# Optimization experiments

Hardware: AMD Instinct MI355X
Metric: run time of the kernel (lower is better)

Reference implementation:

```python
import jax, jax.numpy as jnp
import numpy as np

LOC_SIZE, LOC_EMB = 50000, 512
TIM_SIZE, TIM_EMB = 48, 32
UID_SIZE, UID_EMB = 10000, 64
HID = 512
H = HID + TIM_EMB  # 544, odeblock / merge width
N_SEG = 8192
TOTAL = 262144  # sum(history_count)
SEQ = 1024
TLEN = 1024


def setup_inputs() -> dict:
    key = jax.random.key(0)
    ks = jax.random.split(key, 12)
    # history_count: positive ints summing exactly to TOTAL
    rs = np.random.RandomState(0)
    counts = np.full(N_SEG, TOTAL // N_SEG, dtype=np.int32)  # 32 each
    d = rs.randint(0, 16, N_SEG // 2).astype(np.int32)
    counts[: N_SEG // 2] += d
    counts[N_SEG // 2 :] -= d  # min 17, sum preserved
    return {
        "loc": jax.random.randint(ks[0], (SEQ, 1), 0, LOC_SIZE, dtype=jnp.int32),
        "tim": jax.random.randint(ks[1], (SEQ, 1), 0, TIM_SIZE, dtype=jnp.int32),
        "history_loc": jax.random.randint(ks[2], (TOTAL, 1), 0, LOC_SIZE, dtype=jnp.int32),
        "history_tim": jax.random.randint(ks[3], (TOTAL, 1), 0, TIM_SIZE, dtype=jnp.int32),
        "history_count": jnp.asarray(counts),
        "uid": jax.random.randint(ks[4], (1,), 0, UID_SIZE, dtype=jnp.int32),
        "target_len": TLEN,
        "emb_loc_w": jax.random.normal(ks[5], (LOC_SIZE, LOC_EMB), jnp.float32) * 0.02,
        "emb_tim_w": jax.random.normal(ks[6], (TIM_SIZE, TIM_EMB), jnp.float32) * 0.02,
        "emb_uid_w": jax.random.normal(ks[7], (UID_SIZE, UID_EMB), jnp.float32) * 0.02,
        "gru_w": jax.random.normal(ks[8], (3, H, H), jnp.float32) * (1.0 / np.sqrt(H)),
        "gru_b": jnp.zeros((3, H), jnp.float32),
        "fc_final_w": jax.random.normal(ks[9], (H + UID_EMB, LOC_SIZE), jnp.float32) * 0.02,
        "fc_final_b": jnp.zeros((LOC_SIZE,), jnp.float32),
    }


def reference(loc, tim, history_loc, history_tim, history_count, uid, target_len,
              emb_loc_w, emb_tim_w, emb_uid_w, gru_w, gru_b, fc_final_w, fc_final_b):
    # ----- short-term sequence: embed, concat, dot-attention (Attn method='dot') -----
    x = jnp.concatenate([emb_loc_w[loc[:, 0]], emb_tim_w[tim[:, 0]]], axis=-1)  # [S, H]
    x = x[-target_len:]
    attn_w = jax.nn.softmax(x @ x.T, axis=-1)          # vectorized double-loop of Attn
    x_attn = attn_w @ x                                # [T, H]

    # ----- long-term history: variable-length segment mean (the python loop) -----
    loc_eh = emb_loc_w[history_loc[:, 0]]              # [TOTAL, LOC_EMB]
    tim_eh = emb_tim_w[history_tim[:, 0]]              # [TOTAL, TIM_EMB]
    csum = jnp.cumsum(history_count)                   # inclusive offsets
    offsets = csum - history_count                     # segment starts
    seg_ids = jnp.searchsorted(csum, jnp.arange(loc_eh.shape[0]), side="right")
    loc_mean = jax.ops.segment_sum(loc_eh, seg_ids, num_segments=history_count.shape[0])
    loc_mean = loc_mean / history_count[:, None].astype(x.dtype)  # [N_SEG, LOC_EMB]
    tim_first = tim_eh[offsets]                        # first tim of each segment
    history = jnp.concatenate([loc_mean, tim_first], axis=1)      # [N_SEG, H]

    # ----- merge, autonomous GRU-ODE block (single Euler step, dt=1) -----
    h = jnp.concatenate([history, x_attn], axis=0)     # [N_SEG+T, H]
    r = jax.nn.sigmoid(h @ gru_w[0] + gru_b[0])
    z = jax.nn.sigmoid(h @ gru_w[1] + gru_b[1])
    g = jnp.tanh((r * h) @ gru_w[2] + gru_b[2])
    out_state = h + (1.0 - z) * (g - h)                # h + dh (GRU-ODE derivative)

    # ----- output head -----
    out = out_state[-target_len:]
    uid_emb = jnp.broadcast_to(emb_uid_w[uid[0]], (target_len, emb_uid_w.shape[1]))
    y = jnp.concatenate([out, uid_emb], axis=1) @ fc_final_w + fc_final_b  # [T, V]
    return jax.nn.log_softmax(y, axis=-1)
```

## Files before the change

### kernel.cpp

```cpp
#include <hip/hip_runtime.h>
#include <hip/hip_bf16.h>
#include <math.h>

#define SEQ   1024
#define TL    1024
#define DLOC  512
#define DTIM  32
#define DH    544
#define DUID  64
#define DF    608
#define NVOC  50000
#define NT_FINAL 391
#define NPAD  50048

typedef __attribute__((ext_vector_type(8))) short short8;
typedef __attribute__((ext_vector_type(4))) float f32x4;
typedef __attribute__((ext_vector_type(4))) unsigned short u16x4;

#define WAITV8 asm volatile("s_waitcnt vmcnt(8)" ::: "memory")
#define WAITV4 asm volatile("s_waitcnt vmcnt(4)" ::: "memory")
#define WAITV0 asm volatile("s_waitcnt vmcnt(0)" ::: "memory")

__device__ __forceinline__ unsigned short f2bf(float f) {
    union { float f; unsigned int u; } x; x.f = f;
    unsigned int u = x.u;
    return (unsigned short)((u + 0x7fffu + ((u >> 16) & 1u)) >> 16);
}

__device__ __forceinline__ void gll16(const unsigned short* g, unsigned short* l) {
    __builtin_amdgcn_global_load_lds(
        (const __attribute__((address_space(1))) void*)g,
        (__attribute__((address_space(3))) void*)l,
        16, 0, 0);
}

enum { EPI_S = 0, EPI_PV = 1, EPI_G1 = 2, EPI_G2 = 3 };

template<int EPI>
__global__ __launch_bounds__(256) void gemm_p(
    const unsigned short* __restrict__ A,
    const unsigned short* __restrict__ Bt,
    int K, int N, int lda, int ldo,
    float* __restrict__ o1, unsigned short* __restrict__ o2,
    const float* __restrict__ p1, const float* __restrict__ p2,
    const float* __restrict__ p3, const float* __restrict__ p4)
{
    __shared__ __align__(16) unsigned short SMEM[32768];
    const int m0 = blockIdx.y << 7, n0 = blockIdx.x << 7;
    const int tid = threadIdx.x, w = tid >> 6, lane = tid & 63;
    const int wr = (w >> 1) << 6, wc = (w & 1) << 6;
    const int llo = lane & 15, lhi = lane >> 4;

    const int ch0 = (w * 2 + 0) * 64 + lane;
    const int ch1 = (w * 2 + 1) * 64 + lane;
    const int r0 = ch0 >> 2, s0 = (ch0 & 3) ^ ((r0 >> 1) & 3);
    const int r1 = ch1 >> 2, s1 = (ch1 & 3) ^ ((r1 >> 1) & 3);

    f32x4 acc[4][4];
    #pragma unroll
    for (int i = 0; i < 4; ++i)
        #pragma unroll
        for (int j = 0; j < 4; ++j)
            #pragma unroll
            for (int q = 0; q < 4; ++q) acc[i][j][q] = 0.0f;

    auto STAGE = [&](int buf, int kt) {
        const int k0 = kt << 5;
        unsigned short* As = &SMEM[buf * 4096];
        unsigned short* Bs = &SMEM[16384 + buf * 4096];
        gll16(&A [(size_t)(m0 + r0) * lda + k0 + s0 * 8], &As[(w * 2 + 0) * 512]);
        gll16(&A [(size_t)(m0 + r1) * lda + k0 + s1 * 8], &As[(w * 2 + 1) * 512]);
        gll16(&Bt[(size_t)(n0 + r0) * K   + k0 + s0 * 8], &Bs[(w * 2 + 0) * 512]);
        gll16(&Bt[(size_t)(n0 + r1) * K   + k0 + s1 * 8], &Bs[(w * 2 + 1) * 512]);
    };

    const int nk = K >> 5;
    STAGE(0, 0); STAGE(1, 1); STAGE(2, 2);
    WAITV8;
    __builtin_amdgcn_s_barrier();

    for (int t = 0; t < nk; ++t) {
        const unsigned short* As = &SMEM[(t & 3) * 4096];
        const unsigned short* Bs = &SMEM[16384 + (t & 3) * 4096];
        short8 af[4], bfv[4];
        #pragma unroll
        for (int fm = 0; fm < 4; ++fm) {
            int row = wr + fm * 16 + llo;
            af[fm] = *reinterpret_cast<const short8*>(&As[row * 32 + (lhi ^ ((row >> 1) & 3)) * 8]);
        }
        #pragma unroll
        for (int fn = 0; fn < 4; ++fn) {
            int row = wc + fn * 16 + llo;
            bfv[fn] = *reinterpret_cast<const short8*>(&Bs[row * 32 + (lhi ^ ((row >> 1) & 3)) * 8]);
        }
        if (t + 3 < nk) STAGE((t + 3) & 3, t + 3);
        __builtin_amdgcn_s_setprio(1);
        #pragma unroll
        for (int fm = 0; fm < 4; ++fm)
            #pragma unroll
            for (int fn = 0; fn < 4; ++fn)
                acc[fm][fn] = __builtin_amdgcn_mfma_f32_16x16x32_bf16(af[fm], bfv[fn], acc[fm][fn], 0, 0, 0);
        __builtin_amdgcn_s_setprio(0);
        if (t + 1 < nk) {
            if (t + 3 < nk)      WAITV8;
            else if (t + 2 < nk) WAITV4;
            else                 WAITV0;
            __builtin_amdgcn_s_barrier();
        }
    }

    #pragma unroll
    for (int fm = 0; fm < 4; ++fm)
        #pragma unroll
        for (int fn = 0; fn < 4; ++fn)
            #pragma unroll
            for (int j = 0; j < 4; ++j) {
                int row = m0 + wr + fm * 16 + (lhi << 2) + j;
                int col = n0 + wc + fn * 16 + llo;
                float v = acc[fm][fn][j];
                if (EPI == EPI_S) {
                    if (col < N) o1[(size_t)row * ldo + col] = v;
                } else if (EPI == EPI_PV) {
                    if (col < N) {
                        o1[(size_t)row * ldo + col] = v;
                        o2[(size_t)row * ldo + col] = f2bf(v);
                    }
                } else if (EPI == EPI_G1) {
                    if (col < DH) {
                        float rg = 1.0f / (1.0f + __expf(-(v + p1[col])));
                        o2[(size_t)row * ldo + col] = f2bf(rg * p2[(size_t)row * DH + col]);
                    } else if (col < N) {
                        o1[(size_t)row * ldo + (col - DH)] = v;
                    }
                } else {
                    if (col < N) {
                        float z = 1.0f / (1.0f + __expf(-(p3[(size_t)row * DH + col] + p1[col])));
                        float g = tanhf(v + p2[col]);
                        float h = p4[(size_t)row * DH + col];
                        o2[(size_t)row * ldo + col] = f2bf(h + (1.0f - z) * (g - h));
                    }
                }
            }
}

template<int PASS>
__global__ __launch_bounds__(256) void gemm_fin(
    const unsigned short* __restrict__ Ab,
    const unsigned short* __restrict__ Wt,
    const float* __restrict__ bias,
    float* __restrict__ Y,
    float* __restrict__ Psum,
    const float* __restrict__ LSE)
{
    __shared__ __align__(16) unsigned short SMEM[32768];
    const int bid = blockIdx.x;
    const int wid = (bid & 7) * NT_FINAL + (bid >> 3);
    const int mt = wid & 7, nt = wid >> 3;
    const int m0 = mt << 7, n0 = nt << 7;

    const int tid = threadIdx.x, w = tid >> 6, lane = tid & 63;
    const int wr = (w >> 1) << 6, wc = (w & 1) << 6;
    const int llo = lane & 15, lhi = lane >> 4;

    const int ch0 = (w * 2 + 0) * 64 + lane;
    const int ch1 = (w * 2 + 1) * 64 + lane;
    const int r0 = ch0 >> 2, s0 = (ch0 & 3) ^ ((r0 >> 1) & 3);
    const int r1 = ch1 >> 2, s1 = (ch1 & 3) ^ ((r1 >> 1) & 3);

    f32x4 acc[4][4];
    #pragma unroll
    for (int i = 0; i < 4; ++i)
        #pragma unroll
        for (int j = 0; j < 4; ++j)
            #pragma unroll
            for (int q = 0; q < 4; ++q) acc[i][j][q] = 0.0f;

    auto STAGE = [&](int buf, int kt) {
        const int k0 = kt << 5;
        unsigned short* As = &SMEM[buf * 4096];
        unsigned short* Bs = &SMEM[16384 + buf * 4096];
        gll16(&Ab[(size_t)(m0 + r0) * DF + k0 + s0 * 8], &As[(w * 2 + 0) * 512]);
        gll16(&Ab[(size_t)(m0 + r1) * DF + k0 + s1 * 8], &As[(w * 2 + 1) * 512]);
        gll16(&Wt[(size_t)(n0 + r0) * DF + k0 + s0 * 8], &Bs[(w * 2 + 0) * 512]);
        gll16(&Wt[(size_t)(n0 + r1) * DF + k0 + s1 * 8], &Bs[(w * 2 + 1) * 512]);
    };

    const int nk = DF >> 5;
    STAGE(0, 0); STAGE(1, 1); STAGE(2, 2);
    WAITV8;
    __builtin_amdgcn_s_barrier();

    for (int t = 0; t < nk; ++t) {
        const unsigned short* As = &SMEM[(t & 3) * 4096];
        const unsigned short* Bs = &SMEM[16384 + (t & 3) * 4096];
        short8 af[4], bfv[4];
        #pragma unroll
        for (int fm = 0; fm < 4; ++fm) {
            int row = wr + fm * 16 + llo;
            af[fm] = *reinterpret_cast<const short8*>(&As[row * 32 + (lhi ^ ((row >> 1) & 3)) * 8]);
        }
        #pragma unroll
        for (int fn = 0; fn < 4; ++fn) {
            int row = wc + fn * 16 + llo;
            bfv[fn] = *reinterpret_cast<const short8*>(&Bs[row * 32 + (lhi ^ ((row >> 1) & 3)) * 8]);
        }
        if (t + 3 < nk) STAGE((t + 3) & 3, t + 3);
        __builtin_amdgcn_s_setprio(1);
        #pragma unroll
        for (int fm = 0; fm < 4; ++fm)
            #pragma unroll
            for (int fn = 0; fn < 4; ++fn)
                acc[fm][fn] = __builtin_amdgcn_mfma_f32_16x16x32_bf16(af[fm], bfv[fn], acc[fm][fn], 0, 0, 0);
        __builtin_amdgcn_s_setprio(0);
        if (t + 1 < nk) {
            if (t + 3 < nk)      WAITV8;
            else if (t + 2 < nk) WAITV4;
            else                 WAITV0;
            __builtin_amdgcn_s_barrier();
        }
    }

    if (PASS == 1) {
        __syncthreads();
        float* red = (float*)SMEM;
        #pragma unroll
        for (int fm = 0; fm < 4; ++fm)
            #pragma unroll
            for (int j = 0; j < 4; ++j) {
                int rowl = wr + fm * 16 + (lhi << 2) + j;
                float s = 0.0f;
                #pragma unroll
                for (int fn = 0; fn < 4; ++fn) {
                    int col = n0 + wc + fn * 16 + llo;
                    if (col < NVOC) s += __expf(acc[fm][fn][j] + bias[col]);
                }
                red[rowl * 33 + (wc >> 6) * 16 + llo] = s;
            }
        __syncthreads();
        if (tid < 128) {
            float t2 = 0.0f;
            #pragma unroll
            for (int i = 0; i < 32; ++i) t2 += red[tid * 33 + i];
            Psum[(size_t)(m0 + tid) * NT_FINAL + nt] = t2;
        }
    } else {
        #pragma unroll
        for (int fm = 0; fm < 4; ++fm)
            #pragma unroll
            for (int j = 0; j < 4; ++j) {
                int rowl = wr + fm * 16 + (lhi << 2) + j;
                float l = LSE[m0 + rowl];
                #pragma unroll
                for (int fn = 0; fn < 4; ++fn) {
                    int col = n0 + wc + fn * 16 + llo;
                    if (col < NVOC)
                        Y[(size_t)(m0 + rowl) * NVOC + col] = acc[fm][fn][j] + bias[col] - l;
                }
            }
    }
}

__global__ __launch_bounds__(64) void k_combine(
    const float* __restrict__ Psum, float* __restrict__ LSE)
{
    int r = blockIdx.x, lane = threadIdx.x;
    float s = 0.0f;
    for (int i = lane; i < NT_FINAL; i += 64) s += Psum[(size_t)r * NT_FINAL + i];
    #pragma unroll
    for (int off = 32; off >= 1; off >>= 1) s += __shfl_xor(s, off);
    if (lane == 0) LSE[r] = logf(s);
}

__global__ __launch_bounds__(256) void k_cvtW(
    const float* __restrict__ W, unsigned short* __restrict__ Wt)
{
    __shared__ unsigned short T[64][65];
    const int n0 = blockIdx.x * 64, k0 = blockIdx.y * 64;
    const int tid = threadIdx.x;
    #pragma unroll
    for (int i = 0; i < 4; ++i) {
        int idx = i * 256 + tid;
        int kk = idx >> 4;
        int nq = (idx & 15) << 2;
        int gk = k0 + kk, gn = n0 + nq;
        float4 v;
        if (gk < DF && gn < NVOC) v = *reinterpret_cast<const float4*>(&W[(size_t)gk * NVOC + gn]);
        else { v.x = v.y = v.z = v.w = 0.0f; }
        T[nq + 0][kk] = f2bf(v.x); T[nq + 1][kk] = f2bf(v.y);
        T[nq + 2][kk] = f2bf(v.z); T[nq + 3][kk] = f2bf(v.w);
    }
    __syncthreads();
    #pragma unroll
    for (int i = 0; i < 4; ++i) {
        int idx = i * 256 + tid;
        int nn = idx >> 4;
        int kq = (idx & 15) << 2;
        int gk = k0 + kq;
        if (gk < DF) {
            u16x4 o; o[0] = T[nn][kq]; o[1] = T[nn][kq + 1]; o[2] = T[nn][kq + 2]; o[3] = T[nn][kq + 3];
            *reinterpret_cast<u16x4*>(&Wt[(size_t)(n0 + nn) * DF + gk]) = o;
        }
    }
}

__global__ __launch_bounds__(256) void k_cvtT(
    const float* __restrict__ src, unsigned short* __restrict__ dst,
    int Kdim, int Nvalid, int srcLd)
{
    __shared__ unsigned short T[64][65];
    const int n0 = blockIdx.x * 64, k0 = blockIdx.y * 64;
    const int tid = threadIdx.x;
    #pragma unroll
    for (int i = 0; i < 16; ++i) {
        int idx = i * 256 + tid;
        int kk = idx >> 6, nn = idx & 63;
        int gk = k0 + kk, gn = n0 + nn;
        float v = (gk < Kdim && gn < Nvalid) ? src[(size_t)gk * srcLd + gn] : 0.0f;
        T[nn][kk] = f2bf(v);
    }
    __syncthreads();
    #pragma unroll
    for (int i = 0; i < 16; ++i) {
        int idx = i * 256 + tid;
        int nn = idx >> 6, kk = idx & 63;
        int gk = k0 + kk;
        if (gk < Kdim) dst[(size_t)(n0 + nn) * Kdim + gk] = T[nn][kk];
    }
}

__global__ __launch_bounds__(256) void k_cvtT2(
    const unsigned short* __restrict__ src, unsigned short* __restrict__ dst,
    int Rdim, int Cvalid, int srcLd)
{
    __shared__ unsigned short T[64][65];
    const int c0 = blockIdx.x * 64, r0 = blockIdx.y * 64;
    const int tid = threadIdx.x;
    #pragma unroll
    for (int i = 0; i < 16; ++i) {
        int idx = i * 256 + tid;
        int rr = idx >> 6, cc = idx & 63;
        int gc = c0 + cc;
        T[cc][rr] = (gc < Cvalid) ? src[(size_t)(r0 + rr) * srcLd + gc] : (unsigned short)0;
    }
    __syncthreads();
    #pragma unroll
    for (int i = 0; i < 16; ++i) {
        int idx = i * 256 + tid;
        int cc = idx >> 6, rr = idx & 63;
        dst[(size_t)(c0 + cc) * Rdim + r0 + rr] = T[cc][rr];
    }
}

__global__ __launch_bounds__(256) void k_build_x(
    const int* __restrict__ loc, const int* __restrict__ tim,
    const float* __restrict__ eloc, const float* __restrict__ etim,
    unsigned short* __restrict__ Xb)
{
    int r = blockIdx.x;
    int li = loc[r], ti = tim[r];
    for (int c = threadIdx.x; c < DH; c += 256) {
        float v = (c < DLOC) ? eloc[(size_t)li * DLOC + c]
                             : etim[(size_t)ti * DTIM + (c - DLOC)];
        Xb[(size_t)r * DH + c] = f2bf(v);
    }
}

__global__ __launch_bounds__(256) void k_softmax(
    const float* __restrict__ S, unsigned short* __restrict__ Pb)
{
    int r = blockIdx.x;
    const float* row = S + (size_t)r * SEQ;
    int tid = threadIdx.x;
    float v[4];
    float m = -INFINITY;
    #pragma unroll
    for (int i = 0; i < 4; ++i) { v[i] = row[tid + i * 256]; m = fmaxf(m, v[i]); }
    #pragma unroll
    for (int off = 32; off >= 1; off >>= 1) m = fmaxf(m, __shfl_xor(m, off));
    __shared__ float red[8];
    int w = tid >> 6;
    if ((tid & 63) == 0) red[w] = m;
    __syncthreads();
    m = fmaxf(fmaxf(red[0], red[1]), fmaxf(red[2], red[3]));
    float s = 0.0f;
    #pragma unroll
    for (int i = 0; i < 4; ++i) { v[i] = __expf(v[i] - m); s += v[i]; }
    #pragma unroll
    for (int off = 32; off >= 1; off >>= 1) s += __shfl_xor(s, off);
    __syncthreads();
    if ((tid & 63) == 0) red[4 + w] = s;
    __syncthreads();
    s = red[4] + red[5] + red[6] + red[7];
    float inv = 1.0f / s;
    #pragma unroll
    for (int i = 0; i < 4; ++i)
        Pb[(size_t)r * SEQ + tid + i * 256] = f2bf(v[i] * inv);
}

__global__ __launch_bounds__(256) void k_uid_b(
    const int* __restrict__ uid, const float* __restrict__ euid,
    unsigned short* __restrict__ Ab)
{
    int idx = blockIdx.x * 256 + threadIdx.x;
    if (idx >= TL * DUID) return;
    int r = idx >> 6, c = idx & 63;
    Ab[(size_t)r * DF + DH + c] = f2bf(euid[(size_t)uid[0] * DUID + c]);
}

extern "C" void kernel_launch(void* const* d_in, const int* in_sizes, int n_in,
                              void* d_out, int out_size, void* d_ws, size_t ws_size,
                              hipStream_t stream)
{
    const int*   loc  = (const int*)d_in[0];
    const int*   tim  = (const int*)d_in[1];
    const int*   uid  = (const int*)d_in[5];
    const float* eloc = (const float*)d_in[7];
    const float* etim = (const float*)d_in[8];
    const float* euid = (const float*)d_in[9];
    const float* gru_w = (const float*)d_in[10];
    const float* gru_b = (const float*)d_in[11];
    const float* fcw  = (const float*)d_in[12];
    const float* fcb  = (const float*)d_in[13];
    float* Y = (float*)d_out;

    const float* b0 = gru_b;
    const float* b1 = gru_b + DH;
    const float* b2 = gru_b + 2 * DH;

    float* S    = (float*)d_ws;
    float* Hf   = S    + (size_t)SEQ * SEQ;
    float* A01z = Hf   + (size_t)TL * DH;
    float* Psum = A01z + (size_t)TL * DH;
    float* LSE  = Psum + (size_t)TL * NT_FINAL;
    unsigned short* Xb   = (unsigned short*)(LSE + 1024);
    unsigned short* Xt   = Xb   + (size_t)TL * DH;
    unsigned short* Pb   = Xt   + (size_t)640 * 1024;
    unsigned short* Hb   = Pb   + (size_t)SEQ * SEQ;
    unsigned short* RHb  = Hb   + (size_t)TL * DH;
    unsigned short* Ab   = RHb  + (size_t)TL * DH;
    unsigned short* W01t = Ab   + (size_t)TL * DF;
    unsigned short* W2t  = W01t + (size_t)1184 * DH;
    unsigned short* Wt   = W2t  + (size_t)640 * DH;

    k_cvtW<<<dim3(NPAD / 64, 10), 256, 0, stream>>>(fcw, Wt);
    k_cvtT<<<dim3(9, 9),  256, 0, stream>>>(gru_w,                     W01t,                   DH, DH, DH);
    k_cvtT<<<dim3(10, 9), 256, 0, stream>>>(gru_w + (size_t)DH * DH,   W01t + (size_t)DH * DH, DH, DH, DH);
    k_cvtT<<<dim3(10, 9), 256, 0, stream>>>(gru_w + 2*(size_t)DH * DH, W2t,                    DH, DH, DH);

    k_build_x<<<TL, 256, 0, stream>>>(loc, tim, eloc, etim, Xb);
    k_cvtT2<<<dim3(10, 16), 256, 0, stream>>>(Xb, Xt, TL, DH, DH);

    gemm_p<EPI_S><<<dim3(8, 8), 256, 0, stream>>>(
        Xb, Xb, DH, SEQ, DH, SEQ, S, nullptr, nullptr, nullptr, nullptr, nullptr);
    k_softmax<<<SEQ, 256, 0, stream>>>(S, Pb);
    gemm_p<EPI_PV><<<dim3(5, 8), 256, 0, stream>>>(
        Pb, Xt, SEQ, DH, SEQ, DH, Hf, Hb, nullptr, nullptr, nullptr, nullptr);

    gemm_p<EPI_G1><<<dim3(9, 8), 256, 0, stream>>>(
        Hb, W01t, DH, 1088, DH, DH, A01z, RHb, b0, Hf, nullptr, nullptr);
    gemm_p<EPI_G2><<<dim3(5, 8), 256, 0, stream>>>(
        RHb, W2t, DH, DH, DH, DF, nullptr, Ab, b1, b2, A01z, Hf);
    k_uid_b<<<(TL * DUID + 255) / 256, 256, 0, stream>>>(uid, euid, Ab);

    gemm_fin<1><<<8 * NT_FINAL, 256, 0, stream>>>(Ab, Wt, fcb, Y, Psum, nullptr);
    k_combine<<<TL, 64, 0, stream>>>(Psum, LSE);
    gemm_fin<2><<<8 * NT_FINAL, 256, 0, stream>>>(Ab, Wt, fcb, Y, Psum, LSE);
}
```

Measured before the change: 720.0 us.

## Merge prep kernels into one launch and compute the final GEMM once with a subtract pass

The weight conversion, embedding build, transpose and uid fill kernels are merged into a single k_prep launch. The two-pass final GEMM, which recomputed the full vocabulary product to apply the log-sum-exp, is replaced by one 128x256-tile GEMM. That GEMM writes the biased logits and the partial exp-sums together, and a separate elementwise k_sub pass then subtracts the LSE. This removes a full recompute of the large output GEMM and several launches. In exchange, the large output buffer is now read and written a second time, and the final GEMM drops from 4-stage to double-buffered pipelining.

```diff
diff --git a/kernel.cpp b/kernel.cpp
--- a/kernel.cpp
+++ b/kernel.cpp
@@ -10,16 +10,12 @@
 #define DUID  64
 #define DF    608
 #define NVOC  50000
-#define NT_FINAL 391
-#define NPAD  50048
+#define NT2   196
+#define NPAD2 50176
 
 typedef __attribute__((ext_vector_type(8))) short short8;
 typedef __attribute__((ext_vector_type(4))) float f32x4;
 typedef __attribute__((ext_vector_type(4))) unsigned short u16x4;
-
-#define WAITV8 asm volatile("s_waitcnt vmcnt(8)" ::: "memory")
-#define WAITV4 asm volatile("s_waitcnt vmcnt(4)" ::: "memory")
-#define WAITV0 asm volatile("s_waitcnt vmcnt(0)" ::: "memory")
 
 __device__ __forceinline__ unsigned short f2bf(float f) {
     union { float f; unsigned int u; } x; x.f = f;
@@ -33,6 +29,10 @@
         (__attribute__((address_space(3))) void*)l,
         16, 0, 0);
 }
+
+#define WAITV8 asm volatile("s_waitcnt vmcnt(8)" ::: "memory")
+#define WAITV4 asm volatile("s_waitcnt vmcnt(4)" ::: "memory")
+#define WAITV0 asm volatile("s_waitcnt vmcnt(0)" ::: "memory")
 
 enum { EPI_S = 0, EPI_PV = 1, EPI_G1 = 2, EPI_G2 = 3 };
 
@@ -143,120 +143,107 @@
             }
 }
 
-template<int PASS>
-__global__ __launch_bounds__(256) void gemm_fin(
+__global__ __launch_bounds__(256) void gemm_final3(
     const unsigned short* __restrict__ Ab,
     const unsigned short* __restrict__ Wt,
     const float* __restrict__ bias,
-    float* __restrict__ Y,
-    float* __restrict__ Psum,
-    const float* __restrict__ LSE)
-{
-    __shared__ __align__(16) unsigned short SMEM[32768];
+    float* __restrict__ Y, float* __restrict__ Psum)
+{
+    __shared__ __align__(16) unsigned short SMEM[24576];
     const int bid = blockIdx.x;
-    const int wid = (bid & 7) * NT_FINAL + (bid >> 3);
-    const int mt = wid & 7, nt = wid >> 3;
-    const int m0 = mt << 7, n0 = nt << 7;
+    const int T = (bid & 7) * NT2 + (bid >> 3);
+    const int mt = T & 7, nt = T >> 3;
+    const int m0 = mt << 7, n0 = nt << 8;
 
     const int tid = threadIdx.x, w = tid >> 6, lane = tid & 63;
-    const int wr = (w >> 1) << 6, wc = (w & 1) << 6;
+    const int wr = (w >> 1) << 6;
+    const int wc = (w & 1) << 7;
     const int llo = lane & 15, lhi = lane >> 4;
 
-    const int ch0 = (w * 2 + 0) * 64 + lane;
-    const int ch1 = (w * 2 + 1) * 64 + lane;
-    const int r0 = ch0 >> 2, s0 = (ch0 & 3) ^ ((r0 >> 1) & 3);
-    const int r1 = ch1 >> 2, s1 = (ch1 & 3) ^ ((r1 >> 1) & 3);
-
-    f32x4 acc[4][4];
+    int rA[2], sA[2], rB[4], sB[4];
+    #pragma unroll
+    for (int i = 0; i < 2; ++i) {
+        int f = (w * 2 + i) * 64 + lane;
+        rA[i] = f >> 2; sA[i] = (f & 3) ^ ((rA[i] >> 1) & 3);
+    }
+    #pragma unroll
+    for (int i = 0; i < 4; ++i) {
+        int f = (w * 4 + i) * 64 + lane;
+        rB[i] = f >> 2; sB[i] = (f & 3) ^ ((rB[i] >> 1) & 3);
+    }
+
+    f32x4 acc[4][8];
     #pragma unroll
     for (int i = 0; i < 4; ++i)
         #pragma unroll
-        for (int j = 0; j < 4; ++j)
+        for (int j = 0; j < 8; ++j)
             #pragma unroll
             for (int q = 0; q < 4; ++q) acc[i][j][q] = 0.0f;
 
     auto STAGE = [&](int buf, int kt) {
         const int k0 = kt << 5;
         unsigned short* As = &SMEM[buf * 4096];
-        unsigned short* Bs = &SMEM[16384 + buf * 4096];
-        gll16(&Ab[(size_t)(m0 + r0) * DF + k0 + s0 * 8], &As[(w * 2 + 0) * 512]);
-        gll16(&Ab[(size_t)(m0 + r1) * DF + k0 + s1 * 8], &As[(w * 2 + 1) * 512]);
-        gll16(&Wt[(size_t)(n0 + r0) * DF + k0 + s0 * 8], &Bs[(w * 2 + 0) * 512]);
-        gll16(&Wt[(size_t)(n0 + r1) * DF + k0 + s1 * 8], &Bs[(w * 2 + 1) * 512]);
+        unsigned short* Bs = &SMEM[8192 + buf * 8192];
+        #pragma unroll
+        for (int i = 0; i < 2; ++i)
+            gll16(&Ab[(size_t)(m0 + rA[i]) * DF + k0 + sA[i] * 8], &As[(w * 2 + i) * 512]);
+        #pragma unroll
+        for (int i = 0; i < 4; ++i)
+            gll16(&Wt[(size_t)(n0 + rB[i]) * DF + k0 + sB[i] * 8], &Bs[(w * 4 + i) * 512]);
     };
 
     const int nk = DF >> 5;
-    STAGE(0, 0); STAGE(1, 1); STAGE(2, 2);
-    WAITV8;
-    __builtin_amdgcn_s_barrier();
-
+    STAGE(0, 0);
+    __syncthreads();
     for (int t = 0; t < nk; ++t) {
-        const unsigned short* As = &SMEM[(t & 3) * 4096];
-        const unsigned short* Bs = &SMEM[16384 + (t & 3) * 4096];
-        short8 af[4], bfv[4];
+        if (t + 1 < nk) STAGE((t + 1) & 1, t + 1);
+        const unsigned short* As = &SMEM[(t & 1) * 4096];
+        const unsigned short* Bs = &SMEM[8192 + (t & 1) * 8192];
+        short8 af[4], bfv[8];
         #pragma unroll
         for (int fm = 0; fm < 4; ++fm) {
             int row = wr + fm * 16 + llo;
             af[fm] = *reinterpret_cast<const short8*>(&As[row * 32 + (lhi ^ ((row >> 1) & 3)) * 8]);
         }
         #pragma unroll
-        for (int fn = 0; fn < 4; ++fn) {
+        for (int fn = 0; fn < 8; ++fn) {
             int row = wc + fn * 16 + llo;
             bfv[fn] = *reinterpret_cast<const short8*>(&Bs[row * 32 + (lhi ^ ((row >> 1) & 3)) * 8]);
         }
-        if (t + 3 < nk) STAGE((t + 3) & 3, t + 3);
         __builtin_amdgcn_s_setprio(1);
         #pragma unroll
         for (int fm = 0; fm < 4; ++fm)
             #pragma unroll
-            for (int fn = 0; fn < 4; ++fn)
+            for (int fn = 0; fn < 8; ++fn)
                 acc[fm][fn] = __builtin_amdgcn_mfma_f32_16x16x32_bf16(af[fm], bfv[fn], acc[fm][fn], 0, 0, 0);
         __builtin_amdgcn_s_setprio(0);
-        if (t + 1 < nk) {
-            if (t + 3 < nk)      WAITV8;
-            else if (t + 2 < nk) WAITV4;
-            else                 WAITV0;
-            __builtin_amdgcn_s_barrier();
-        }
-    }
-
-    if (PASS == 1) {
         __syncthreads();
-        float* red = (float*)SMEM;
-        #pragma unroll
-        for (int fm = 0; fm < 4; ++fm)
-            #pragma unroll
-            for (int j = 0; j < 4; ++j) {
-                int rowl = wr + fm * 16 + (lhi << 2) + j;
-                float s = 0.0f;
-                #pragma unroll
-                for (int fn = 0; fn < 4; ++fn) {
-                    int col = n0 + wc + fn * 16 + llo;
-                    if (col < NVOC) s += __expf(acc[fm][fn][j] + bias[col]);
-                }
-                red[rowl * 33 + (wc >> 6) * 16 + llo] = s;
-            }
-        __syncthreads();
-        if (tid < 128) {
-            float t2 = 0.0f;
-            #pragma unroll
-            for (int i = 0; i < 32; ++i) t2 += red[tid * 33 + i];
-            Psum[(size_t)(m0 + tid) * NT_FINAL + nt] = t2;
-        }
-    } else {
-        #pragma unroll
-        for (int fm = 0; fm < 4; ++fm)
-            #pragma unroll
-            for (int j = 0; j < 4; ++j) {
-                int rowl = wr + fm * 16 + (lhi << 2) + j;
-                float l = LSE[m0 + rowl];
-                #pragma unroll
-                for (int fn = 0; fn < 4; ++fn) {
-                    int col = n0 + wc + fn * 16 + llo;
-                    if (col < NVOC)
-                        Y[(size_t)(m0 + rowl) * NVOC + col] = acc[fm][fn][j] + bias[col] - l;
+    }
+
+    float* red = (float*)SMEM;
+    #pragma unroll
+    for (int fm = 0; fm < 4; ++fm)
+        #pragma unroll
+        for (int j = 0; j < 4; ++j) {
+            int rowl = wr + fm * 16 + (lhi << 2) + j;
+            float s = 0.0f;
+            #pragma unroll
+            for (int fn = 0; fn < 8; ++fn) {
+                int col = n0 + wc + fn * 16 + llo;
+                if (col < NVOC) {
+                    float v = acc[fm][fn][j] + bias[col];
+                    Y[(size_t)(m0 + rowl) * NVOC + col] = v;
+                    s += __expf(v);
                 }
             }
+            red[rowl * 33 + (wc >> 7) * 16 + llo] = s;
+        }
+    __syncthreads();
+    if (tid < 128) {
+        float t2 = 0.0f;
+        #pragma unroll
+        for (int i = 0; i < 32; ++i) t2 += red[tid * 33 + i];
+        Psum[(size_t)(m0 + tid) * NT2 + nt] = t2;
     }
 }
 
@@ -265,58 +252,36 @@
 {
     int r = blockIdx.x, lane = threadIdx.x;
     float s = 0.0f;
-    for (int i = lane; i < NT_FINAL; i += 64) s += Psum[(size_t)r * NT_FINAL + i];
+    for (int i = lane; i < NT2; i += 64) s += Psum[(size_t)r * NT2 + i];
     #pragma unroll
     for (int off = 32; off >= 1; off >>= 1) s += __shfl_xor(s, off);
     if (lane == 0) LSE[r] = logf(s);
 }
 
-__global__ __launch_bounds__(256) void k_cvtW(
-    const float* __restrict__ W, unsigned short* __restrict__ Wt)
-{
-    __shared__ unsigned short T[64][65];
-    const int n0 = blockIdx.x * 64, k0 = blockIdx.y * 64;
-    const int tid = threadIdx.x;
-    #pragma unroll
-    for (int i = 0; i < 4; ++i) {
-        int idx = i * 256 + tid;
-        int kk = idx >> 4;
-        int nq = (idx & 15) << 2;
-        int gk = k0 + kk, gn = n0 + nq;
-        float4 v;
-        if (gk < DF && gn < NVOC) v = *reinterpret_cast<const float4*>(&W[(size_t)gk * NVOC + gn]);
-        else { v.x = v.y = v.z = v.w = 0.0f; }
-        T[nq + 0][kk] = f2bf(v.x); T[nq + 1][kk] = f2bf(v.y);
-        T[nq + 2][kk] = f2bf(v.z); T[nq + 3][kk] = f2bf(v.w);
-    }
-    __syncthreads();
-    #pragma unroll
-    for (int i = 0; i < 4; ++i) {
-        int idx = i * 256 + tid;
-        int nn = idx >> 4;
-        int kq = (idx & 15) << 2;
-        int gk = k0 + kq;
-        if (gk < DF) {
-            u16x4 o; o[0] = T[nn][kq]; o[1] = T[nn][kq + 1]; o[2] = T[nn][kq + 2]; o[3] = T[nn][kq + 3];
-            *reinterpret_cast<u16x4*>(&Wt[(size_t)(n0 + nn) * DF + gk]) = o;
-        }
-    }
-}
-
-__global__ __launch_bounds__(256) void k_cvtT(
-    const float* __restrict__ src, unsigned short* __restrict__ dst,
-    int Kdim, int Nvalid, int srcLd)
-{
-    __shared__ unsigned short T[64][65];
-    const int n0 = blockIdx.x * 64, k0 = blockIdx.y * 64;
-    const int tid = threadIdx.x;
+__global__ __launch_bounds__(256) void k_sub(
+    float* __restrict__ Y, const float* __restrict__ lse)
+{
+    int r = blockIdx.y;
+    int c4 = blockIdx.x * 256 + threadIdx.x;
+    if (c4 >= NVOC / 4) return;
+    float l = lse[r];
+    float4* p = reinterpret_cast<float4*>(Y + (size_t)r * NVOC);
+    float4 v = p[c4];
+    v.x -= l; v.y -= l; v.z -= l; v.w -= l;
+    p[c4] = v;
+}
+
+__device__ __forceinline__ void dev_cvtT(
+    unsigned short* T, const float* __restrict__ src, unsigned short* __restrict__ dst,
+    int Kdim, int Nvalid, int srcLd, int n0, int k0, int tid, int rowCap)
+{
     #pragma unroll
     for (int i = 0; i < 16; ++i) {
         int idx = i * 256 + tid;
         int kk = idx >> 6, nn = idx & 63;
         int gk = k0 + kk, gn = n0 + nn;
         float v = (gk < Kdim && gn < Nvalid) ? src[(size_t)gk * srcLd + gn] : 0.0f;
-        T[nn][kk] = f2bf(v);
+        T[nn * 65 + kk] = f2bf(v);
     }
     __syncthreads();
     #pragma unroll
@@ -324,44 +289,88 @@
         int idx = i * 256 + tid;
         int nn = idx >> 6, kk = idx & 63;
         int gk = k0 + kk;
-        if (gk < Kdim) dst[(size_t)(n0 + nn) * Kdim + gk] = T[nn][kk];
-    }
-}
-
-__global__ __launch_bounds__(256) void k_cvtT2(
-    const unsigned short* __restrict__ src, unsigned short* __restrict__ dst,
-    int Rdim, int Cvalid, int srcLd)
-{
-    __shared__ unsigned short T[64][65];
-    const int c0 = blockIdx.x * 64, r0 = blockIdx.y * 64;
-    const int tid = threadIdx.x;
-    #pragma unroll
-    for (int i = 0; i < 16; ++i) {
-        int idx = i * 256 + tid;
-        int rr = idx >> 6, cc = idx & 63;
-        int gc = c0 + cc;
-        T[cc][rr] = (gc < Cvalid) ? src[(size_t)(r0 + rr) * srcLd + gc] : (unsigned short)0;
-    }
-    __syncthreads();
-    #pragma unroll
-    for (int i = 0; i < 16; ++i) {
-        int idx = i * 256 + tid;
-        int cc = idx >> 6, rr = idx & 63;
-        dst[(size_t)(c0 + cc) * Rdim + r0 + rr] = T[cc][rr];
-    }
-}
-
-__global__ __launch_bounds__(256) void k_build_x(
+        if (gk < Kdim && (n0 + nn) < rowCap)
+            dst[(size_t)(n0 + nn) * Kdim + gk] = T[nn * 65 + kk];
+    }
+}
+
+__global__ __launch_bounds__(256) void k_prep(
+    const float* __restrict__ fcw, const float* __restrict__ gru_w,
     const int* __restrict__ loc, const int* __restrict__ tim,
     const float* __restrict__ eloc, const float* __restrict__ etim,
-    unsigned short* __restrict__ Xb)
-{
-    int r = blockIdx.x;
-    int li = loc[r], ti = tim[r];
-    for (int c = threadIdx.x; c < DH; c += 256) {
-        float v = (c < DLOC) ? eloc[(size_t)li * DLOC + c]
-                             : etim[(size_t)ti * DTIM + (c - DLOC)];
-        Xb[(size_t)r * DH + c] = f2bf(v);
+    const int* __restrict__ uid, const float* __restrict__ euid,
+    unsigned short* __restrict__ Wt, unsigned short* __restrict__ W01t,
+    unsigned short* __restrict__ W2t, unsigned short* __restrict__ Xb,
+    unsigned short* __restrict__ Xt, unsigned short* __restrict__ Ab)
+{
+    __shared__ unsigned short T[64 * 65];
+    const int tid = threadIdx.x;
+    const int b = blockIdx.x;
+
+    if (b < 7840) {
+        const int n0 = (b % 784) << 6, k0 = (b / 784) << 6;
+        #pragma unroll
+        for (int i = 0; i < 4; ++i) {
+            int idx = i * 256 + tid;
+            int kk = idx >> 4;
+            int nq = (idx & 15) << 2;
+            int gk = k0 + kk, gn = n0 + nq;
+            float4 v;
+            if (gk < DF && gn < NVOC) v = *reinterpret_cast<const float4*>(&fcw[(size_t)gk * NVOC + gn]);
+            else { v.x = v.y = v.z = v.w = 0.0f; }
+            T[(nq + 0) * 65 + kk] = f2bf(v.x); T[(nq + 1) * 65 + kk] = f2bf(v.y);
+            T[(nq + 2) * 65 + kk] = f2bf(v.z); T[(nq + 3) * 65 + kk] = f2bf(v.w);
+        }
+        __syncthreads();
+        #pragma unroll
+        for (int i = 0; i < 4; ++i) {
+            int idx = i * 256 + tid;
+            int nn = idx >> 4;
+            int kq = (idx & 15) << 2;
+            int gk = k0 + kq;
+            if (gk < DF) {
+                u16x4 o; o[0] = T[nn * 65 + kq]; o[1] = T[nn * 65 + kq + 1];
+                o[2] = T[nn * 65 + kq + 2]; o[3] = T[nn * 65 + kq + 3];
+                *reinterpret_cast<u16x4*>(&Wt[(size_t)(n0 + nn) * DF + gk]) = o;
+            }
+        }
+    } else if (b < 7921) {
+        int lb = b - 7840;
+        dev_cvtT(T, gru_w, W01t, DH, DH, DH, (lb % 9) << 6, (lb / 9) << 6, tid, DH);
+    } else if (b < 8011) {
+        int lb = b - 7921;
+        dev_cvtT(T, gru_w + (size_t)DH * DH, W01t + (size_t)DH * DH,
+                 DH, DH, DH, (lb % 10) << 6, (lb / 10) << 6, tid, 640);
+    } else if (b < 8101) {
+        int lb = b - 8011;
+        dev_cvtT(T, gru_w + 2 * (size_t)DH * DH, W2t,
+                 DH, DH, DH, (lb % 10) << 6, (lb / 10) << 6, tid, 640);
+    } else if (b < 8261) {
+        int lb = b - 8101;
+        const int c0 = (lb % 10) << 6, r0 = (lb / 10) << 6;
+        #pragma unroll
+        for (int i = 0; i < 16; ++i) {
+            int idx = i * 256 + tid;
+            int rr = idx >> 6, cc = idx & 63;
+            int r = r0 + rr, c = c0 + cc;
+            float v = 0.0f;
+            if (c < DLOC)       v = eloc[(size_t)loc[r] * DLOC + c];
+            else if (c < DH)    v = etim[(size_t)tim[r] * DTIM + (c - DLOC)];
+            unsigned short bv = f2bf(v);
+            T[cc * 65 + rr] = bv;
+            if (c < DH) Xb[(size_t)r * DH + c] = bv;
+        }
+        __syncthreads();
+        #pragma unroll
+        for (int i = 0; i < 16; ++i) {
+            int idx = i * 256 + tid;
+            int cc = idx >> 6, rr = idx & 63;
+            Xt[(size_t)(c0 + cc) * TL + r0 + rr] = T[cc * 65 + rr];
+        }
+    } else {
+        int idx = (b - 8261) * 256 + tid;
+        int r = idx >> 6, c = idx & 63;
+        Ab[(size_t)r * DF + DH + c] = f2bf(euid[(size_t)uid[0] * DUID + c]);
     }
 }
 
@@ -395,16 +404,6 @@
     #pragma unroll
     for (int i = 0; i < 4; ++i)
         Pb[(size_t)r * SEQ + tid + i * 256] = f2bf(v[i] * inv);
-}
-
-__global__ __launch_bounds__(256) void k_uid_b(
-    const int* __restrict__ uid, const float* __restrict__ euid,
-    unsigned short* __restrict__ Ab)
-{
-    int idx = blockIdx.x * 256 + threadIdx.x;
-    if (idx >= TL * DUID) return;
-    int r = idx >> 6, c = idx & 63;
-    Ab[(size_t)r * DF + DH + c] = f2bf(euid[(size_t)uid[0] * DUID + c]);
 }
 
 extern "C" void kernel_launch(void* const* d_in, const int* in_sizes, int n_in,
@@ -431,7 +430,7 @@
     float* Hf   = S    + (size_t)SEQ * SEQ;
     float* A01z = Hf   + (size_t)TL * DH;
     float* Psum = A01z + (size_t)TL * DH;
-    float* LSE  = Psum + (size_t)TL * NT_FINAL;
+    float* LSE  = Psum + (size_t)TL * NT2;
     unsigned short* Xb   = (unsigned short*)(LSE + 1024);
     unsigned short* Xt   = Xb   + (size_t)TL * DH;
     unsigned short* Pb   = Xt   + (size_t)640 * 1024;
@@ -442,13 +441,8 @@
     unsigned short* W2t  = W01t + (size_t)1184 * DH;
     unsigned short* Wt   = W2t  + (size_t)640 * DH;
 
-    k_cvtW<<<dim3(NPAD / 64, 10), 256, 0, stream>>>(fcw, Wt);
-    k_cvtT<<<dim3(9, 9),  256, 0, stream>>>(gru_w,                     W01t,                   DH, DH, DH);
-    k_cvtT<<<dim3(10, 9), 256, 0, stream>>>(gru_w + (size_t)DH * DH,   W01t + (size_t)DH * DH, DH, DH, DH);
-    k_cvtT<<<dim3(10, 9), 256, 0, stream>>>(gru_w + 2*(size_t)DH * DH, W2t,                    DH, DH, DH);
-
-    k_build_x<<<TL, 256, 0, stream>>>(loc, tim, eloc, etim, Xb);
-    k_cvtT2<<<dim3(10, 16), 256, 0, stream>>>(Xb, Xt, TL, DH, DH);
+    k_prep<<<8517, 256, 0, stream>>>(fcw, gru_w, loc, tim, eloc, etim, uid, euid,
+                                     Wt, W01t, W2t, Xb, Xt, Ab);
 
     gemm_p<EPI_S><<<dim3(8, 8), 256, 0, stream>>>(
         Xb, Xb, DH, SEQ, DH, SEQ, S, nullptr, nullptr, nullptr, nullptr, nullptr);
@@ -460,9 +454,8 @@
         Hb, W01t, DH, 1088, DH, DH, A01z, RHb, b0, Hf, nullptr, nullptr);
     gemm_p<EPI_G2><<<dim3(5, 8), 256, 0, stream>>>(
         RHb, W2t, DH, DH, DH, DF, nullptr, Ab, b1, b2, A01z, Hf);
-    k_uid_b<<<(TL * DUID + 255) / 256, 256, 0, stream>>>(uid, euid, Ab);
-
-    gemm_fin<1><<<8 * NT_FINAL, 256, 0, stream>>>(Ab, Wt, fcb, Y, Psum, nullptr);
+
+    gemm_final3<<<8 * NT2, 256, 0, stream>>>(Ab, Wt, fcb, Y, Psum);
     k_combine<<<TL, 64, 0, stream>>>(Psum, LSE);
-    gemm_fin<2><<<8 * NT_FINAL, 256, 0, stream>>>(Ab, Wt, fcb, Y, Psum, LSE);
-}
+    k_sub<<<dim3((NVOC / 4 + 255) / 256, TL), 256, 0, stream>>>(Y, LSE);
+}
```

New measurement: 755.1 us. 1.05x slower.
